# Kernel optimization log

Hardware: AMD Instinct MI355X
Metric: run time of the kernel (lower is better)

Reference implementation:

```python
import jax, jax.numpy as jnp
import numpy as np

SL, BS, E, H, PF, STRIDE, SHIFT = 2048, 2, 1024, 16, 16, 1, 0
DH = E // H  # 64


def setup_inputs() -> dict:
    key = jax.random.key(0)
    ks = jax.random.split(key, 6)
    s = 0.02
    return {
        'x': jax.random.normal(ks[0], (SL, BS, E), jnp.float32),
        'ln_g': jnp.ones((E,), jnp.float32),
        'ln_b': jnp.zeros((E,), jnp.float32),
        'Wq': jax.random.normal(ks[1], (E, E), jnp.float32) * s,
        'bq': jnp.zeros((E,), jnp.float32),
        'Wk': jax.random.normal(ks[2], (E, E), jnp.float32) * s,
        'bk': jnp.zeros((E,), jnp.float32),
        'Wv': jax.random.normal(ks[3], (E, E), jnp.float32) * s,
        'bv': jnp.zeros((E,), jnp.float32),
        'Wo': jax.random.normal(ks[4], (E, E), jnp.float32) * s,
        'bo': jnp.zeros((E,), jnp.float32),
    }


def _layernorm(x, g, b, eps=1e-5):
    m = x.mean(-1, keepdims=True)
    v = jnp.var(x, axis=-1, keepdims=True)
    return (x - m) * jax.lax.rsqrt(v + eps) * g + b


def _sparsify(context, h):
    # faithful to sparsify(): r = (arange(h)+1)*stride - pf + shift (+ arange(pf)), mod c
    c = context.shape[0]
    base = (jnp.arange(h) + 1) * STRIDE - PF + SHIFT          # [h]
    idx = (base[None, :] + jnp.arange(PF)[:, None]) % c       # [pf, h]
    return context[idx.reshape(-1)].reshape(PF, h, context.shape[1], context.shape[2])


def reference(x, ln_g, ln_b, Wq, bq, Wk, bk, Wv, bv, Wo, bo):
    sl, bs, e = x.shape
    residual = x
    xn = _layernorm(x, ln_g, ln_b)
    # gather pf-sized local context window per query position (modular wrap)
    fetch = _sparsify(xn, sl)                                  # [pf, sl, bs, E]
    # per-token query (length-1) attending to its pf gathered keys
    q = (xn @ Wq + bq).reshape(sl, bs, H, DH)                  # [sl,bs,H,dh]
    k = (fetch @ Wk + bk).reshape(PF, sl, bs, H, DH)           # [pf,sl,bs,H,dh]
    v = (fetch @ Wv + bv).reshape(PF, sl, bs, H, DH)
    scale = 1.0 / jnp.sqrt(jnp.float32(DH))
    scores = jnp.einsum('sbhd,psbhd->sbhp', q, k) * scale      # [sl,bs,H,pf]
    attn = jax.nn.softmax(scores, axis=-1)
    out = jnp.einsum('sbhp,psbhd->sbhd', attn, v).reshape(sl, bs, e)
    out = out @ Wo + bo                                        # output projection
    # dropout is a no-op in eval
    return residual + out
```

## Files before the change

kernel.cpp:

```cpp
#include <hip/hip_runtime.h>
#include <cstdint>
#include <cstddef>

#define SLEN 2048
#define BSZ  2
#define EDIM 1024
#define NHEAD 16
#define DHEAD 64
#define PFW  16
#define NTOK (SLEN*BSZ)

typedef __attribute__((ext_vector_type(8))) short short8;
typedef __attribute__((ext_vector_type(4))) float floatx4;
typedef __attribute__((ext_vector_type(4))) int   int4v;

__device__ __forceinline__ short f2bf(float f) {
  union { float f; uint32_t u; } v; v.f = f;
  uint32_t r = v.u + 0x7fffu + ((v.u >> 16) & 1u);
  return (short)(r >> 16);
}
__device__ __forceinline__ float bf2f(short s) {
  union { uint32_t u; float f; } v; v.u = ((uint32_t)(uint16_t)s) << 16;
  return v.f;
}
__device__ __forceinline__ int q8(float f, float inv) {
  int q = __float2int_rn(f * inv);
  return min(127, max(-127, q));
}

__device__ __forceinline__ void async16(const void* g, void* l) {
  __builtin_amdgcn_global_load_lds((const __attribute__((address_space(1))) void*)g,
                                   (__attribute__((address_space(3))) void*)l,
                                   16, 0, 0);
}

#define VMCNT(n) asm volatile("s_waitcnt vmcnt(" #n ")" ::: "memory")

__global__ __launch_bounds__(256) void prep_kernel(
    const float* __restrict__ x, const float* __restrict__ g,
    const float* __restrict__ b, char* __restrict__ xn_i8,
    float* __restrict__ xn_scl,
    const float* __restrict__ W0, const float* __restrict__ W1,
    const float* __restrict__ W2, const float* __restrict__ W3,
    short* __restrict__ Wt_base)
{
  const int bid = blockIdx.x;
  const int tid = threadIdx.x;

  if (bid < NTOK) {
    const int row = bid;
    const float4 v = ((const float4*)(x + (size_t)row * EDIM))[tid];
    float s  = v.x + v.y + v.z + v.w;
    float ss = v.x * v.x + v.y * v.y + v.z * v.z + v.w * v.w;
#pragma unroll
    for (int off = 32; off; off >>= 1) {
      s  += __shfl_xor(s, off);
      ss += __shfl_xor(ss, off);
    }
    __shared__ float ws_s[4], ws_ss[4], ws_m[4];
    const int lane = tid & 63, wave = tid >> 6;
    if (lane == 0) { ws_s[wave] = s; ws_ss[wave] = ss; }
    __syncthreads();
    s  = ws_s[0] + ws_s[1] + ws_s[2] + ws_s[3];
    ss = ws_ss[0] + ws_ss[1] + ws_ss[2] + ws_ss[3];

    const float mean = s * (1.0f / EDIM);
    const float var  = ss * (1.0f / EDIM) - mean * mean;
    const float rs   = rsqrtf(var + 1e-5f);

    const float4 gv = ((const float4*)g)[tid];
    const float4 bv = ((const float4*)b)[tid];
    const float n0 = (v.x - mean) * rs * gv.x + bv.x;
    const float n1 = (v.y - mean) * rs * gv.y + bv.y;
    const float n2 = (v.z - mean) * rs * gv.z + bv.z;
    const float n3 = (v.w - mean) * rs * gv.w + bv.w;

    float am = fmaxf(fmaxf(fabsf(n0), fabsf(n1)), fmaxf(fabsf(n2), fabsf(n3)));
#pragma unroll
    for (int off = 32; off; off >>= 1) am = fmaxf(am, __shfl_xor(am, off));
    if (lane == 0) ws_m[wave] = am;
    __syncthreads();
    am = fmaxf(fmaxf(ws_m[0], ws_m[1]), fmaxf(ws_m[2], ws_m[3]));

    const float inv = (am > 1e-30f) ? 127.0f / am : 0.0f;
    const int q0 = q8(n0, inv), q1 = q8(n1, inv), q2 = q8(n2, inv), q3 = q8(n3, inv);
    const uint32_t pack = (uint32_t)(q0 & 0xff) | ((uint32_t)(q1 & 0xff) << 8) |
                          ((uint32_t)(q2 & 0xff) << 16) | ((uint32_t)(q3 & 0xff) << 24);
    ((uint32_t*)(xn_i8 + (size_t)row * EDIM))[tid] = pack;
    if (tid == 0) xn_scl[row] = am * (1.0f / 127.0f);
  } else {
    const int t = bid - NTOK;
    const int z = t >> 10;
    const int rem = t & 1023;
    const int n0 = (rem & 31) * 32;
    const int k0 = (rem >> 5) * 32;
    const float* W = (z == 0) ? W0 : (z == 1) ? W1 : (z == 2) ? W2 : W3;
    short* Wt = Wt_base + (size_t)z * EDIM * EDIM;

    __shared__ float tile[32][33];
    const int tx = tid & 31;
    const int ty = tid >> 5;
#pragma unroll
    for (int i = 0; i < 4; ++i)
      tile[ty + i * 8][tx] = W[(size_t)(k0 + ty + i * 8) * EDIM + n0 + tx];
    __syncthreads();
#pragma unroll
    for (int i = 0; i < 4; ++i)
      Wt[(size_t)(n0 + ty + i * 8) * EDIM + k0 + tx] = f2bf(tile[tx][ty + i * 8]);
  }
}

__global__ __launch_bounds__(256) void quant_w(
    const short* __restrict__ Wt, char* __restrict__ w_i8,
    float* __restrict__ w_scl)
{
  const int R = blockIdx.x;
  const int tid = threadIdx.x;
  const short4 s4 = ((const short4*)(Wt + (size_t)R * EDIM))[tid];
  const float w0 = bf2f(s4.x), w1 = bf2f(s4.y), w2 = bf2f(s4.z), w3 = bf2f(s4.w);

  float am = fmaxf(fmaxf(fabsf(w0), fabsf(w1)), fmaxf(fabsf(w2), fabsf(w3)));
#pragma unroll
  for (int off = 32; off; off >>= 1) am = fmaxf(am, __shfl_xor(am, off));
  __shared__ float wm[4];
  const int lane = tid & 63, wave = tid >> 6;
  if (lane == 0) wm[wave] = am;
  __syncthreads();
  am = fmaxf(fmaxf(wm[0], wm[1]), fmaxf(wm[2], wm[3]));

  const float inv = (am > 1e-30f) ? 127.0f / am : 0.0f;
  const int q0 = q8(w0, inv), q1 = q8(w1, inv), q2 = q8(w2, inv), q3 = q8(w3, inv);
  const uint32_t pack = (uint32_t)(q0 & 0xff) | ((uint32_t)(q1 & 0xff) << 8) |
                        ((uint32_t)(q2 & 0xff) << 16) | ((uint32_t)(q3 & 0xff) << 24);
  ((uint32_t*)(w_i8 + (size_t)R * EDIM))[tid] = pack;
  if (tid == 0) w_scl[R] = am * (1.0f / 127.0f);
}

__global__ __launch_bounds__(512, 2) void gemm_qkv256(
    const char* __restrict__ xn_i8, const float* __restrict__ xn_scl,
    const char* __restrict__ w_i8, const float* __restrict__ w_scl,
    const float* __restrict__ bq, const float* __restrict__ bk,
    const float* __restrict__ bv, short* __restrict__ qkv_base)
{
  __shared__ __align__(16) char lds[4][32768];

  const int bid = blockIdx.x;
  const int lin = (bid & 7) * 24 + (bid >> 3);
  const int mt  = lin & 15;
  const int nt  = lin >> 4;
  const int z   = nt >> 2;
  const int bm  = mt * 256;
  const int bnz = (nt & 3) * 256;

  const float* bias = (z == 0) ? bq : (z == 1) ? bk : bv;
  short* out = qkv_base + (size_t)z * NTOK * EDIM;

  const int tid = threadIdx.x;
  const int wv  = tid >> 6;
  const int ln  = tid & 63;
  const int q   = ln >> 4;
  const int l16 = ln & 15;
  const int wm  = wv >> 2;
  const int wn  = wv & 3;

  const int sr = tid >> 2;
  const int sc = ((tid & 3) * 16) ^ ((sr & 3) * 16);
  const char* gA0 = xn_i8 + (size_t)(bm + sr) * EDIM + sc;
  const char* gA1 = gA0 + (size_t)128 * EDIM;
  const char* gB0 = w_i8 + ((size_t)z << 20) + (size_t)(bnz + sr) * EDIM + sc;
  const char* gB1 = gB0 + (size_t)128 * EDIM;
  const int wbase = wv * 1024;

#define QSTAGE(tt) do { \
    char* s_ = lds[(tt) & 3]; \
    async16(gA0 + (tt) * 64, s_ + wbase); \
    async16(gA1 + (tt) * 64, s_ + 8192 + wbase); \
    async16(gB0 + (tt) * 64, s_ + 16384 + wbase); \
    async16(gB1 + (tt) * 64, s_ + 24576 + wbase); \
  } while (0)

  const int swz  = (q * 16) ^ ((l16 & 3) * 16);
  const int aoff = (wm * 128 + l16) * 64 + swz;
  const int boff = 16384 + (wn * 64 + l16) * 64 + swz;

  int4v acc[8][4];
#pragma unroll
  for (int mi = 0; mi < 8; ++mi)
#pragma unroll
    for (int ni = 0; ni < 4; ++ni) { int4v zz = {0, 0, 0, 0}; acc[mi][ni] = zz; }

  QSTAGE(0); QSTAGE(1); QSTAGE(2);
  VMCNT(8);
  __builtin_amdgcn_s_barrier();
  __builtin_amdgcn_sched_barrier(0);

#pragma unroll
  for (int t = 0; t < 16; ++t) {
    if (t + 3 < 16) QSTAGE(t + 3);

    const char* sl = lds[t & 3];
    int4v bf[4], af[8];
#pragma unroll
    for (int ni = 0; ni < 4; ++ni)
      bf[ni] = *(const int4v*)(sl + boff + ni * 1024);
#pragma unroll
    for (int mi = 0; mi < 8; ++mi)
      af[mi] = *(const int4v*)(sl + aoff + mi * 1024);

    __builtin_amdgcn_s_setprio(1);
#pragma unroll
    for (int mi = 0; mi < 8; ++mi)
#pragma unroll
      for (int ni = 0; ni < 4; ++ni)
        acc[mi][ni] = __builtin_amdgcn_mfma_i32_16x16x64_i8(
            af[mi], bf[ni], acc[mi][ni], 0, 0, 0);
    __builtin_amdgcn_s_setprio(0);

    if (t < 15) {
      if (t <= 12)      VMCNT(8);
      else if (t == 13) VMCNT(4);
      else              VMCNT(0);
      __builtin_amdgcn_s_barrier();
      __builtin_amdgcn_sched_barrier(0);
    }
  }
#undef QSTAGE

  const int rbase = bm + wm * 128 + q * 4;
  const int cbl   = bnz + wn * 64 + l16;
#pragma unroll
  for (int mi = 0; mi < 8; ++mi) {
    float sa[4];
#pragma unroll
    for (int r = 0; r < 4; ++r) sa[r] = xn_scl[rbase + mi * 16 + r];
#pragma unroll
    for (int ni = 0; ni < 4; ++ni) {
      const int c  = cbl + ni * 16;
      const float sb = w_scl[z * EDIM + c];
      const float bb = bias[c];
      const int4v v = acc[mi][ni];
#pragma unroll
      for (int r = 0; r < 4; ++r)
        out[(size_t)(rbase + mi * 16 + r) * EDIM + c] =
            f2bf((float)v[r] * (sa[r] * sb) + bb);
    }
  }
}

__global__ __launch_bounds__(256) void gemm_o_i8(
    const char* __restrict__ A8, const float* __restrict__ a_scl,
    const char* __restrict__ w_i8, const float* __restrict__ w_scl,
    const float* __restrict__ bo, const float* __restrict__ residual,
    float* __restrict__ out)
{
  __shared__ __align__(16) char As[64 * 64];
  __shared__ __align__(16) char Bs[128 * 64];
  __shared__ float sa_lds[64 * 17];

  const int bm = blockIdx.x * 64;
  const int bn = blockIdx.y * 128;
  const int tid  = threadIdx.x;
  const int lane = tid & 63;
  const int wave = tid >> 6;

#pragma unroll
  for (int i = 0; i < 4; ++i) {
    const int e = tid + i * 256;
    const int row = e >> 4, h = e & 15;
    sa_lds[row * 17 + h] = a_scl[(size_t)(bm + row) * NHEAD + h];
  }

  floatx4 facc[2][4];
#pragma unroll
  for (int i = 0; i < 2; ++i)
#pragma unroll
    for (int j = 0; j < 4; ++j) { floatx4 zz = {0.f, 0.f, 0.f, 0.f}; facc[i][j] = zz; }

  const int lrow  = lane >> 2;
  const int lcolB = (lane & 3) * 16;
  const char* gA0 = A8 + (size_t)(bm + wave * 16 + lrow) * EDIM + lcolB;
  const char* gB0 = w_i8 + (size_t)3 * EDIM * EDIM +
                    (size_t)(bn + wave * 32 + lrow) * EDIM + lcolB;
  const char* gB1 = gB0 + (size_t)16 * EDIM;
  char* lA0 = As + wave * 1024;
  char* lB0 = Bs + wave * 2048;
  char* lB1 = lB0 + 1024;

  const int wm  = (wave >> 1) * 32;
  const int wn  = (wave & 1) * 64;
  const int fr  = lane & 15;
  const int fqB = (lane >> 4) * 16;
  const int q4  = lane >> 4;

  for (int ki = 0; ki < 16; ++ki) {
    async16(gA0, lA0);
    async16(gB0, lB0); async16(gB1, lB1);
    gA0 += 64; gB0 += 64; gB1 += 64;
    __syncthreads();

    int4v af[2], bf[4];
#pragma unroll
    for (int mi = 0; mi < 2; ++mi)
      af[mi] = *(const int4v*)(As + (size_t)(wm + mi * 16 + fr) * 64 + fqB);
#pragma unroll
    for (int ni = 0; ni < 4; ++ni)
      bf[ni] = *(const int4v*)(Bs + (size_t)(wn + ni * 16 + fr) * 64 + fqB);

    float sa_v[2][4];
#pragma unroll
    for (int mi = 0; mi < 2; ++mi)
#pragma unroll
      for (int r = 0; r < 4; ++r)
        sa_v[mi][r] = sa_lds[(wm + mi * 16 + q4 * 4 + r) * 17 + ki];

#pragma unroll
    for (int mi = 0; mi < 2; ++mi)
#pragma unroll
      for (int ni = 0; ni < 4; ++ni) {
        const int4v zz = {0, 0, 0, 0};
        const int4v t = __builtin_amdgcn_mfma_i32_16x16x64_i8(
            af[mi], bf[ni], zz, 0, 0, 0);
#pragma unroll
        for (int r = 0; r < 4; ++r)
          facc[mi][ni][r] += sa_v[mi][r] * (float)t[r];
      }
    __syncthreads();
  }

  const int r0 = bm + wm + q4 * 4;
  const int c0 = bn + wn + (lane & 15);
#pragma unroll
  for (int mi = 0; mi < 2; ++mi)
#pragma unroll
    for (int ni = 0; ni < 4; ++ni) {
      const int col = c0 + ni * 16;
      const float sb = w_scl[3 * EDIM + col];
      const float bb = bo[col];
#pragma unroll
      for (int r = 0; r < 4; ++r) {
        const int row = r0 + mi * 16 + r;
        const size_t idx = (size_t)row * EDIM + col;
        out[idx] = residual[idx] + facc[mi][ni][r] * sb + bb;
      }
    }
}

#define VT_LD 80
#define PB_LD 40

__global__ __launch_bounds__(256) void attn_mfma(
    const short* __restrict__ Q, const short* __restrict__ K,
    const short* __restrict__ V, char* __restrict__ O8,
    float* __restrict__ a_scl)
{
  const int tid  = threadIdx.x;
  const int lane = tid & 63;
  const int wave = tid >> 6;
  const int quad = lane >> 4;
  const int l16  = lane & 15;

  const int bh = blockIdx.y;
  const int h  = bh & (NHEAD - 1);
  const int b  = bh >> 4;
  const int s_blk = blockIdx.x * 64;
  const int col0  = h * DHEAD;

  __shared__ __align__(16) short VT[64 * VT_LD];
  __shared__ __align__(16) short Pb[4][16 * PB_LD];

  for (int task = tid; task < 320; task += 256) {
    const int kp  = task >> 3;
    const int dg  = task & 7;
    const int kk0 = kp * 2;
    int sA = s_blk - 15 + kk0;
    int sB = sA + 1;
    if (sA < 0) sA += SLEN;  if (sA >= SLEN) sA -= SLEN;
    if (sB < 0) sB += SLEN;  if (sB >= SLEN) sB -= SLEN;
    const short8 vA = *(const short8*)(V + (size_t)(sA * BSZ + b) * EDIM + col0 + dg * 8);
    const short8 vB = *(const short8*)(V + (size_t)(sB * BSZ + b) * EDIM + col0 + dg * 8);
#pragma unroll
    for (int j = 0; j < 8; ++j) {
      const int d = dg * 8 + j;
      const uint32_t pack = (uint32_t)(uint16_t)vA[j] | ((uint32_t)(uint16_t)vB[j] << 16);
      *(uint32_t*)&VT[d * VT_LD + kk0] = pack;
    }
  }

  const int sw = s_blk + wave * 16;
  short8 aq[2];
  {
    const size_t base = (size_t)((sw + l16) * BSZ + b) * EDIM + col0 + quad * 8;
    aq[0] = *(const short8*)(Q + base);
    aq[1] = *(const short8*)(Q + base + 32);
  }
  short8 bkf[2][2];
#pragma unroll
  for (int T = 0; T < 2; ++T) {
    int ks = sw - 15 + T * 16 + l16;
    if (ks < 0) ks += SLEN;
    if (ks >= SLEN) ks -= SLEN;
    const size_t base = (size_t)(ks * BSZ + b) * EDIM + col0 + quad * 8;
    bkf[T][0] = *(const short8*)(K + base);
    bkf[T][1] = *(const short8*)(K + base + 32);
  }

  floatx4 S[2];
  { floatx4 zz = {0.f, 0.f, 0.f, 0.f}; S[0] = zz; S[1] = zz; }
#pragma unroll
  for (int T = 0; T < 2; ++T) {
    S[T] = __builtin_amdgcn_mfma_f32_16x16x32_bf16(aq[0], bkf[T][0], S[T], 0, 0, 0);
    S[T] = __builtin_amdgcn_mfma_f32_16x16x32_bf16(aq[1], bkf[T][1], S[T], 0, 0, 0);
  }

  float sc[2][4];
#pragma unroll
  for (int T = 0; T < 2; ++T)
#pragma unroll
    for (int r = 0; r < 4; ++r) {
      const int m = quad * 4 + r;
      const int c = T * 16 + l16;
      const int d = c - m;
      sc[T][r] = (d >= 0 && d <= 15) ? S[T][r] * 0.125f : -1e30f;
    }
  float mx[4], sm[4];
#pragma unroll
  for (int r = 0; r < 4; ++r) mx[r] = fmaxf(sc[0][r], sc[1][r]);
#pragma unroll
  for (int off = 1; off <= 8; off <<= 1)
#pragma unroll
    for (int r = 0; r < 4; ++r) mx[r] = fmaxf(mx[r], __shfl_xor(mx[r], off));
  float p[2][4];
#pragma unroll
  for (int r = 0; r < 4; ++r) {
    p[0][r] = __expf(sc[0][r] - mx[r]);
    p[1][r] = __expf(sc[1][r] - mx[r]);
    sm[r] = p[0][r] + p[1][r];
  }
#pragma unroll
  for (int off = 1; off <= 8; off <<= 1)
#pragma unroll
    for (int r = 0; r < 4; ++r) sm[r] += __shfl_xor(sm[r], off);

  __syncthreads();

  short* Pw = Pb[wave];
#pragma unroll
  for (int T = 0; T < 2; ++T)
#pragma unroll
    for (int r = 0; r < 4; ++r) {
      const int m = quad * 4 + r;
      const int c = T * 16 + l16;
      Pw[m * PB_LD + c] = f2bf(p[T][r]);
    }
  __syncthreads();
  const short8 ap = *(const short8*)(Pw + l16 * PB_LD + quad * 8);

  floatx4 Oacc[4];
  { floatx4 zz = {0.f, 0.f, 0.f, 0.f}; Oacc[0] = zz; Oacc[1] = zz; Oacc[2] = zz; Oacc[3] = zz; }
#pragma unroll
  for (int nt = 0; nt < 4; ++nt) {
    const short8 bv = *(const short8*)(VT + (nt * 16 + l16) * VT_LD + wave * 16 + quad * 8);
    Oacc[nt] = __builtin_amdgcn_mfma_f32_16x16x32_bf16(ap, bv, Oacc[nt], 0, 0, 0);
  }

  float vv[4][4];
  float am[4] = {0.f, 0.f, 0.f, 0.f};
#pragma unroll
  for (int nt = 0; nt < 4; ++nt)
#pragma unroll
    for (int r = 0; r < 4; ++r) {
      const float v = Oacc[nt][r] / sm[r];
      vv[nt][r] = v;
      am[r] = fmaxf(am[r], fabsf(v));
    }
#pragma unroll
  for (int off = 1; off <= 8; off <<= 1)
#pragma unroll
    for (int r = 0; r < 4; ++r) am[r] = fmaxf(am[r], __shfl_xor(am[r], off));

  float inv[4];
#pragma unroll
  for (int r = 0; r < 4; ++r) inv[r] = (am[r] > 1e-30f) ? 127.0f / am[r] : 0.0f;

#pragma unroll
  for (int nt = 0; nt < 4; ++nt)
#pragma unroll
    for (int r = 0; r < 4; ++r) {
      const int m = quad * 4 + r;
      const int row = (sw + m) * BSZ + b;
      O8[(size_t)row * EDIM + col0 + nt * 16 + l16] = (char)q8(vv[nt][r], inv[r]);
    }
  if (l16 == 0) {
#pragma unroll
    for (int r = 0; r < 4; ++r) {
      const int m = quad * 4 + r;
      const int row = (sw + m) * BSZ + b;
      a_scl[(size_t)row * NHEAD + h] = am[r] * (1.0f / 127.0f);
    }
  }
}

extern "C" void kernel_launch(void* const* d_in, const int* in_sizes, int n_in,
                              void* d_out, int out_size, void* d_ws, size_t ws_size,
                              hipStream_t stream) {
  const float* x    = (const float*)d_in[0];
  const float* ln_g = (const float*)d_in[1];
  const float* ln_b = (const float*)d_in[2];
  const float* Wq   = (const float*)d_in[3];
  const float* bq   = (const float*)d_in[4];
  const float* Wk   = (const float*)d_in[5];
  const float* bk   = (const float*)d_in[6];
  const float* Wv   = (const float*)d_in[7];
  const float* bv   = (const float*)d_in[8];
  const float* Wo   = (const float*)d_in[9];
  const float* bo   = (const float*)d_in[10];
  float* out = (float*)d_out;

  char* ws = (char*)d_ws;
  char*  xn_i8   = ws;
  short* Wt      = (short*)(ws + ((size_t)4  << 20));
  char*  w_i8    = ws + ((size_t)12 << 20);
  short* QKV     = (short*)(ws + ((size_t)16 << 20));
  char*  attn_i8 = ws + ((size_t)40 << 20);
  float* xn_scl  = (float*)(ws + ((size_t)44 << 20));
  float* w_scl   = (float*)(ws + ((size_t)44 << 20) + (1 << 16));
  float* a_scl   = (float*)(ws + ((size_t)44 << 20) + (2 << 16));

  prep_kernel<<<NTOK + 4096, 256, 0, stream>>>(x, ln_g, ln_b, xn_i8, xn_scl,
                                               Wq, Wk, Wv, Wo, Wt);
  quant_w<<<4 * EDIM, 256, 0, stream>>>(Wt, w_i8, w_scl);
  gemm_qkv256<<<192, 512, 0, stream>>>(xn_i8, xn_scl, w_i8, w_scl,
                                       bq, bk, bv, QKV);
  attn_mfma<<<dim3(SLEN / 64, BSZ * NHEAD), 256, 0, stream>>>(
      QKV, QKV + (size_t)NTOK * EDIM, QKV + (size_t)2 * NTOK * EDIM,
      attn_i8, a_scl);
  gemm_o_i8<<<dim3(NTOK / 64, EDIM / 128), 256, 0, stream>>>(
      attn_i8, a_scl, w_i8, w_scl, bo, x, out);
}
```

Measured before the change: 151.9 us.

## Pipeline output-projection int8 GEMM with 4-stage async LDS ring buffer

Replaces the single-buffered load-then-sync loop in the output projection GEMM with a 4-slot LDS ring that prefetches three k-tiles ahead using async global-to-LDS copies. Explicit vmcnt waits and one barrier per iteration replace the two __syncthreads calls, so memory latency overlaps with MFMA work. It also raises wave priority around the MFMA block. LDS use grows to 48KB plus scales, which can lower occupancy. The waits depend on the VMCNT macro counts matching the number of outstanding loads.

Result: slower. 177.6 us (+17.0%).

```diff
diff --git a/kernel.cpp b/kernel.cpp
--- a/kernel.cpp
+++ b/kernel.cpp
@@ -253,8 +253,7 @@
     const float* __restrict__ bo, const float* __restrict__ residual,
     float* __restrict__ out)
 {
-  __shared__ __align__(16) char As[64 * 64];
-  __shared__ __align__(16) char Bs[128 * 64];
+  __shared__ __align__(16) char ring[4][12288];
   __shared__ float sa_lds[64 * 17];
 
   const int bm = blockIdx.x * 64;
@@ -282,9 +281,15 @@
   const char* gB0 = w_i8 + (size_t)3 * EDIM * EDIM +
                     (size_t)(bn + wave * 32 + lrow) * EDIM + lcolB;
   const char* gB1 = gB0 + (size_t)16 * EDIM;
-  char* lA0 = As + wave * 1024;
-  char* lB0 = Bs + wave * 2048;
-  char* lB1 = lB0 + 1024;
+  const int aw = wave * 1024;
+  const int bw = 4096 + wave * 2048;
+
+#define OSTAGE(tt) do { \
+    char* s_ = ring[(tt) & 3]; \
+    async16(gA0 + (tt) * 64, s_ + aw); \
+    async16(gB0 + (tt) * 64, s_ + bw); \
+    async16(gB1 + (tt) * 64, s_ + bw + 1024); \
+  } while (0)
 
   const int wm  = (wave >> 1) * 32;
   const int wn  = (wave & 1) * 64;
@@ -292,40 +297,55 @@
   const int fqB = (lane >> 4) * 16;
   const int q4  = lane >> 4;
 
-  for (int ki = 0; ki < 16; ++ki) {
-    async16(gA0, lA0);
-    async16(gB0, lB0); async16(gB1, lB1);
-    gA0 += 64; gB0 += 64; gB1 += 64;
-    __syncthreads();
-
+  OSTAGE(0); OSTAGE(1); OSTAGE(2);
+  VMCNT(6);
+  asm volatile("s_waitcnt lgkmcnt(0)" ::: "memory");
+  __builtin_amdgcn_s_barrier();
+  __builtin_amdgcn_sched_barrier(0);
+
+#pragma unroll
+  for (int t = 0; t < 16; ++t) {
+    if (t + 3 < 16) OSTAGE(t + 3);
+
+    const char* sl = ring[t & 3];
     int4v af[2], bf[4];
 #pragma unroll
     for (int mi = 0; mi < 2; ++mi)
-      af[mi] = *(const int4v*)(As + (size_t)(wm + mi * 16 + fr) * 64 + fqB);
+      af[mi] = *(const int4v*)(sl + (size_t)(wm + mi * 16 + fr) * 64 + fqB);
 #pragma unroll
     for (int ni = 0; ni < 4; ++ni)
-      bf[ni] = *(const int4v*)(Bs + (size_t)(wn + ni * 16 + fr) * 64 + fqB);
+      bf[ni] = *(const int4v*)(sl + 4096 + (size_t)(wn + ni * 16 + fr) * 64 + fqB);
 
     float sa_v[2][4];
 #pragma unroll
     for (int mi = 0; mi < 2; ++mi)
 #pragma unroll
       for (int r = 0; r < 4; ++r)
-        sa_v[mi][r] = sa_lds[(wm + mi * 16 + q4 * 4 + r) * 17 + ki];
-
+        sa_v[mi][r] = sa_lds[(wm + mi * 16 + q4 * 4 + r) * 17 + t];
+
+    __builtin_amdgcn_s_setprio(1);
 #pragma unroll
     for (int mi = 0; mi < 2; ++mi)
 #pragma unroll
       for (int ni = 0; ni < 4; ++ni) {
         const int4v zz = {0, 0, 0, 0};
-        const int4v t = __builtin_amdgcn_mfma_i32_16x16x64_i8(
+        const int4v tt = __builtin_amdgcn_mfma_i32_16x16x64_i8(
             af[mi], bf[ni], zz, 0, 0, 0);
 #pragma unroll
         for (int r = 0; r < 4; ++r)
-          facc[mi][ni][r] += sa_v[mi][r] * (float)t[r];
+          facc[mi][ni][r] += sa_v[mi][r] * (float)tt[r];
       }
-    __syncthreads();
-  }
+    __builtin_amdgcn_s_setprio(0);
+
+    if (t < 15) {
+      if (t <= 12)      VMCNT(6);
+      else if (t == 13) VMCNT(3);
+      else              VMCNT(0);
+      __builtin_amdgcn_s_barrier();
+      __builtin_amdgcn_sched_barrier(0);
+    }
+  }
+#undef OSTAGE
 
   const int r0 = bm + wm + q4 * 4;
   const int c0 = bn + wn + (lane & 15);
```
